# Optimization experiments

Hardware: AMD Instinct MI355X
Metric: run time of the kernel (lower is better)

The kernel has to match this reference:

```python
import jax, jax.numpy as jnp
import numpy as np

D_MODEL = 1024
D_STATE = 64


def setup_inputs() -> dict:
    key = jax.random.key(0)
    k_x, k_a, k_b, k_c, k_d = jax.random.split(key, 5)
    x = jax.random.normal(k_x, (4, 4096, D_MODEL), dtype=jnp.float32)
    # parameter init mirrors _init_parameters
    A_diag = jax.random.uniform(k_a, (D_STATE,), minval=-0.5, maxval=0.5, dtype=jnp.float32)
    def xavier(k, shape):
        fan_in, fan_out = shape
        limit = float(np.sqrt(6.0 / (fan_in + fan_out)))
        return jax.random.uniform(k, shape, minval=-limit, maxval=limit, dtype=jnp.float32)
    B = xavier(k_b, (D_MODEL, D_STATE))
    C = xavier(k_c, (D_STATE, D_MODEL))
    D = xavier(k_d, (D_MODEL, D_MODEL)) * 0.1
    return {"x": x, "A_diag": A_diag, "B": B, "C": C, "D": D}


def reference(x, A_diag, B, C, D):
    # h_t = sigmoid(A_diag) * h_{t-1} + x_t @ B ; y_t = h_t @ C + x_t @ D
    # dropout is identity in eval mode.
    a = jax.nn.sigmoid(A_diag)                      # [S_state]
    u = jnp.einsum('btd,ds->bts', x, B)             # precompute input drive [B,T,S]

    def step(h, u_t):                               # h: [B,S], u_t: [B,S]
        h = a * h + u_t
        return h, h

    h0 = jnp.zeros((x.shape[0], A_diag.shape[0]), dtype=x.dtype)
    _, hs = jax.lax.scan(step, h0, jnp.swapaxes(u, 0, 1))  # hs: [T,B,S]
    hs = jnp.swapaxes(hs, 0, 1)                            # [B,T,S]
    y = jnp.einsum('bts,sd->btd', hs, C) + jnp.einsum('btd,de->bte', x, D)
    return y
```

## Files before the change

kernel.cpp:

```cpp
#include <hip/hip_runtime.h>
#include <hip/hip_bf16.h>

using bf16x8 = __attribute__((ext_vector_type(8))) __bf16;
using f32x4  = __attribute__((ext_vector_type(4))) float;

#define MTOT   16384
#define DMODEL 1024
#define DSTATE 64
#define KBIG   1088

__device__ __forceinline__ ushort f2b(float f) {
  __hip_bfloat16 h = __float2bfloat16(f);
  return *reinterpret_cast<ushort*>(&h);
}

__device__ __forceinline__ void gld_lds16(const ushort* g, const char* l) {
  using gptr_t = const __attribute__((address_space(1))) uint32_t*;
  using lptr_t = __attribute__((address_space(3))) uint32_t*;
  __builtin_amdgcn_global_load_lds(
      reinterpret_cast<gptr_t>(reinterpret_cast<uintptr_t>(g)),
      reinterpret_cast<lptr_t>(static_cast<uint32_t>(reinterpret_cast<uintptr_t>(l))),
      16, 0, 0);
}

#define BARRIER() do { asm volatile("" ::: "memory"); __builtin_amdgcn_s_barrier(); asm volatile("" ::: "memory"); } while (0)
#define VMCNT4() asm volatile("s_waitcnt vmcnt(4)" ::: "memory")
#define VMCNT0() asm volatile("s_waitcnt vmcnt(0)" ::: "memory")

__global__ void prep_params(const float* __restrict__ A_diag, const float* __restrict__ B,
                            const float* __restrict__ C, const float* __restrict__ D,
                            ushort* __restrict__ Wt, ushort* __restrict__ Btu,
                            float* __restrict__ aSig) {
  int i = blockIdx.x * blockDim.x + threadIdx.x;
  int stride = gridDim.x * blockDim.x;
  for (int idx = i; idx < DMODEL * KBIG; idx += stride) {
    int n = idx / KBIG, k = idx % KBIG;
    float v = (k < DSTATE) ? C[k * DMODEL + n] : D[(size_t)(k - DSTATE) * DMODEL + n];
    Wt[idx] = f2b(v);
  }
  for (int idx = i; idx < DSTATE * DMODEL; idx += stride) {
    int s = idx >> 10, k = idx & 1023;
    Btu[idx] = f2b(B[k * DSTATE + s]);
  }
  if (i < DSTATE) aSig[i] = 1.0f / (1.0f + expf(-A_diag[i]));
}

__global__ __launch_bounds__(256) void fused_xu(const float* __restrict__ x,
    const ushort* __restrict__ Btu, const float* __restrict__ aSig,
    ushort* __restrict__ Z, float* __restrict__ Uloc, float* __restrict__ carry) {
  __shared__ ushort As[64][136];
  __shared__ float  Ul[64][68];
  int tid = threadIdx.x;
  int w = tid >> 6, lane = tid & 63;
  int l16 = lane & 15, lh = lane >> 4;
  int row0 = blockIdx.x * 64;

  f32x4 acc[4] = {};
  float4 xv[8];
#pragma unroll
  for (int p = 0; p < 8; ++p) {
    int fi = p * 256 + tid;
    int r = fi >> 5, kq = fi & 31;
    xv[p] = *reinterpret_cast<const float4*>(x + (size_t)(row0 + r) * 1024 + kq * 4);
  }
  for (int c = 0; c < 8; ++c) {
    int k0 = c * 128;
#pragma unroll
    for (int p = 0; p < 8; ++p) {
      int fi = p * 256 + tid;
      int r = fi >> 5, kq = fi & 31;
      ushort4 o;
      o.x = f2b(xv[p].x); o.y = f2b(xv[p].y); o.z = f2b(xv[p].z); o.w = f2b(xv[p].w);
      *reinterpret_cast<ushort4*>(&Z[(size_t)(row0 + r) * KBIG + DSTATE + k0 + kq * 4]) = o;
      *reinterpret_cast<ushort4*>(&As[r][kq * 4]) = o;
    }
    __syncthreads();
    if (c < 7) {
      int k1 = k0 + 128;
#pragma unroll
      for (int p = 0; p < 8; ++p) {
        int fi = p * 256 + tid;
        int r = fi >> 5, kq = fi & 31;
        xv[p] = *reinterpret_cast<const float4*>(x + (size_t)(row0 + r) * 1024 + k1 + kq * 4);
      }
    }
#pragma unroll
    for (int ks = 0; ks < 4; ++ks) {
      bf16x8 af = *reinterpret_cast<const bf16x8*>(&As[w * 16 + l16][ks * 32 + lh * 8]);
#pragma unroll
      for (int n = 0; n < 4; ++n) {
        bf16x8 bf = *reinterpret_cast<const bf16x8*>(
            &Btu[(size_t)(n * 16 + l16) * 1024 + k0 + ks * 32 + lh * 8]);
        acc[n] = __builtin_amdgcn_mfma_f32_16x16x32_bf16(af, bf, acc[n], 0, 0, 0);
      }
    }
    __syncthreads();
  }
#pragma unroll
  for (int n = 0; n < 4; ++n)
#pragma unroll
    for (int j = 0; j < 4; ++j)
      Ul[w * 16 + lh * 4 + j][n * 16 + l16] = acc[n][j];
  __syncthreads();
  int s = lane;
  float as = aSig[s];
  float h = 0.0f;
  int g = blockIdx.x * 4 + w;
#pragma unroll
  for (int i = 0; i < 16; ++i) {
    h = fmaf(as, h, Ul[w * 16 + i][s]);
    Uloc[(size_t)(g * 16 + i) * 64 + s] = h;
  }
  carry[(size_t)g * 64 + s] = h;
}

__global__ __launch_bounds__(256) void carry_scan(const float* __restrict__ aSig,
    const float* __restrict__ carry, float* __restrict__ Hpref) {
  int b = threadIdx.x >> 6, s = threadIdx.x & 63;
  float as = aSig[s];
  float aL = as;
#pragma unroll
  for (int q = 0; q < 4; ++q) aL *= aL;
  const float* cb = carry + ((size_t)b * 256) * 64 + s;
  float* hp = Hpref + ((size_t)b * 256) * 64 + s;
  float H = 0.0f;
  for (int c0 = 0; c0 < 256; c0 += 16) {
    float v[16];
#pragma unroll
    for (int i = 0; i < 16; ++i) v[i] = cb[(size_t)(c0 + i) * 64];
#pragma unroll
    for (int i = 0; i < 16; ++i) {
      hp[(size_t)(c0 + i) * 64] = H;
      H = fmaf(aL, H, v[i]);
    }
  }
}

__global__ __launch_bounds__(256) void scan_fix2(const float* __restrict__ aSig,
    const float* __restrict__ Uloc, const float* __restrict__ Hpref,
    ushort* __restrict__ Z) {
  int w = threadIdx.x >> 6, s = threadIdx.x & 63;
  int g = blockIdx.x * 4 + w;
  float as = aSig[s];
  float H = Hpref[(size_t)g * 64 + s];
  float p = as;
  size_t ubase = (size_t)g * 16 * 64 + s;
  size_t zbase = (size_t)(g * 16) * KBIG + s;
#pragma unroll
  for (int i = 0; i < 16; ++i) {
    float h = fmaf(p, H, Uloc[ubase + (size_t)i * 64]);
    p *= as;
    Z[zbase + (size_t)i * KBIG] = f2b(h);
  }
}

__global__ __launch_bounds__(512) void gemm256(const ushort* __restrict__ A, int lda,
                                               const ushort* __restrict__ Bt, int ldb,
                                               float* __restrict__ Cc, int ldc, int K) {
  extern __shared__ __align__(128) char smem[];
  const int tid = threadIdx.x;
  const int wid = tid >> 6, lane = tid & 63;
  const int wm = wid >> 2, wn = wid & 3;
  const int l16 = lane & 15, lh = lane >> 4;

  int bid = blockIdx.x;
  int swz = (bid & 7) * ((int)gridDim.x >> 3) + (bid >> 3);
  const int bmRow = (swz >> 2) * 256;
  const int bnCol = (swz & 3) * 256;

  const int NT = K / 64;

  const int cswz = ((lh ^ (l16 & 7)) << 4);
  const int sRow = lane >> 3;
  const int sCol = (((lane & 7) ^ (lane >> 3)) << 3);

  f32x4 acc[8][4] = {};
  bf16x8 aR[8], bR[8];

  auto stageA = [&](int buf, int t, int h) {
    size_t r = (size_t)(bmRow + h * 128 + wid * 8 + sRow);
    const ushort* g0 = A + r * (size_t)lda + t * 64 + sCol;
    const char* d = smem + buf * 65536 + (h * 128 + wid * 8) * 128;
    gld_lds16(g0, d);
    gld_lds16(g0 + (size_t)64 * lda, d + 64 * 128);
  };
  auto stageB = [&](int buf, int t, int h) {
    size_t r = (size_t)(bnCol + h * 128 + wid * 8 + sRow);
    const ushort* g0 = Bt + r * (size_t)ldb + t * 64 + sCol;
    const char* d = smem + buf * 65536 + 32768 + (h * 128 + wid * 8) * 128;
    gld_lds16(g0, d);
    gld_lds16(g0 + (size_t)64 * ldb, d + 64 * 128);
  };
  auto loadA = [&](int buf, int qm) {
#pragma unroll
    for (int m = 0; m < 4; ++m)
#pragma unroll
      for (int ks = 0; ks < 2; ++ks)
        aR[m * 2 + ks] = *reinterpret_cast<const bf16x8*>(
            smem + buf * 65536 + (wm * 128 + qm * 64 + m * 16 + l16) * 128 + (cswz ^ (ks * 64)));
  };
  auto loadB = [&](int buf, int qn) {
#pragma unroll
    for (int n = 0; n < 2; ++n)
#pragma unroll
      for (int ks = 0; ks < 2; ++ks)
        bR[qn * 4 + n * 2 + ks] = *reinterpret_cast<const bf16x8*>(
            smem + buf * 65536 + 32768 + (wn * 64 + qn * 32 + n * 16 + l16) * 128 + (cswz ^ (ks * 64)));
  };
  auto mfmaQ = [&](int qm, int qn) {
    __builtin_amdgcn_s_setprio(1);
    __builtin_amdgcn_sched_barrier(0);
#pragma unroll
    for (int ks = 0; ks < 2; ++ks)
#pragma unroll
      for (int m = 0; m < 4; ++m)
#pragma unroll
        for (int n = 0; n < 2; ++n)
          acc[qm * 4 + m][qn * 2 + n] = __builtin_amdgcn_mfma_f32_16x16x32_bf16(
              aR[m * 2 + ks], bR[qn * 4 + n * 2 + ks], acc[qm * 4 + m][qn * 2 + n], 0, 0, 0);
    __builtin_amdgcn_sched_barrier(0);
    __builtin_amdgcn_s_setprio(0);
  };

  stageA(0, 0, 0); stageA(0, 0, 1); stageB(0, 0, 0); stageB(0, 0, 1);
  if (1 < NT) { stageA(1, 1, 0); stageA(1, 1, 1); stageB(1, 1, 0); stageB(1, 1, 1); }
  VMCNT0();
  BARRIER();

  for (int t = 0; t < NT; t += 2) {
    const bool s01 = (t > 0) && (t + 1 < NT);
    const bool s23 = (t + 2 < NT);
    const bool s67 = (t + 3 < NT);
    loadA(0, 0); loadB(0, 0);
    if (s01) stageA(1, t + 1, 0);
    BARRIER(); mfmaQ(0, 0); BARRIER();
    loadB(0, 1);
    if (s01) stageA(1, t + 1, 1);
    BARRIER(); mfmaQ(0, 1); BARRIER();
    loadA(0, 1);
    if (s23) stageB(0, t + 2, 0);
    BARRIER(); mfmaQ(1, 0); BARRIER();
    if (s23) stageB(0, t + 2, 1);
    BARRIER(); mfmaQ(1, 1);
    if (s23) { VMCNT4(); } else { VMCNT0(); }
    BARRIER();
    if (t + 1 < NT) {
      loadA(1, 0); loadB(1, 0);
      if (s23) stageA(0, t + 2, 0);
      BARRIER(); mfmaQ(0, 0); BARRIER();
      loadB(1, 1);
      if (s23) stageA(0, t + 2, 1);
      BARRIER(); mfmaQ(0, 1); BARRIER();
      loadA(1, 1);
      if (s67) stageB(1, t + 3, 0);
      BARRIER(); mfmaQ(1, 0); BARRIER();
      if (s67) stageB(1, t + 3, 1);
      BARRIER(); mfmaQ(1, 1);
      if (s67) { VMCNT4(); } else { VMCNT0(); }
      BARRIER();
    }
  }

#pragma unroll
  for (int i = 0; i < 8; ++i)
#pragma unroll
    for (int jn = 0; jn < 4; ++jn)
#pragma unroll
      for (int j = 0; j < 4; ++j) {
        int r = bmRow + wm * 128 + (i >> 2) * 64 + (i & 3) * 16 + lh * 4 + j;
        int c = bnCol + wn * 64 + (jn >> 1) * 32 + (jn & 1) * 16 + l16;
        Cc[(size_t)r * ldc + c] = acc[i][jn][j];
      }
}

extern "C" void kernel_launch(void* const* d_in, const int* in_sizes, int n_in,
                              void* d_out, int out_size, void* d_ws, size_t ws_size,
                              hipStream_t stream) {
  const float* x      = (const float*)d_in[0];
  const float* A_diag = (const float*)d_in[1];
  const float* B      = (const float*)d_in[2];
  const float* C      = (const float*)d_in[3];
  const float* D      = (const float*)d_in[4];
  float* y = (float*)d_out;

  char* w = (char*)d_ws;
  ushort* Z     = (ushort*)(w);
  ushort* Wt    = (ushort*)(w + 35651584);
  ushort* Btu   = (ushort*)(w + 37879808);
  float*  Uloc  = (float*) (w + 38010880);
  float*  carry = (float*) (w + 42205184);
  float*  Hpref = (float*) (w + 42467328);
  float*  aSig  = (float*) (w + 42729472);

  (void)hipFuncSetAttribute(reinterpret_cast<const void*>(&gemm256),
                            hipFuncAttributeMaxDynamicSharedMemorySize, 131072);

  prep_params<<<dim3(1024), dim3(256), 0, stream>>>(A_diag, B, C, D, Wt, Btu, aSig);
  fused_xu<<<dim3(256), dim3(256), 0, stream>>>(x, Btu, aSig, Z, Uloc, carry);
  carry_scan<<<dim3(1), dim3(256), 0, stream>>>(aSig, carry, Hpref);
  scan_fix2<<<dim3(256), dim3(256), 0, stream>>>(aSig, Uloc, Hpref, Z);
  gemm256<<<dim3(64 * 4), dim3(512), 131072, stream>>>(Z, KBIG, Wt, KBIG, y, DMODEL, KBIG);
}
```

Before: 89.11 us.

## Restructure GEMM main loop with register-double-buffered fragments and fewer barriers

Rewrites the gemm256 main loop as a per-tile routine with two barriers per K-tile instead of about eight. The A and B LDS fragments are double-buffered in registers, so the next tile's fragments load while the current quadrant's MFMAs run. Staging now issues four global-to-LDS loads per operand in one block, the prologue waits only on the first buffer, and the sched_barrier fences are dropped so the compiler can interleave. This costs more VGPRs for the extra fragment buffers. The loop's tail handling assumes an odd tile count (K=1088 gives 17), so an even K would read the wrong buffer in the last tile.

```diff
diff --git a/kernel.cpp b/kernel.cpp
--- a/kernel.cpp
+++ b/kernel.cpp
@@ -24,6 +24,7 @@
 }
 
 #define BARRIER() do { asm volatile("" ::: "memory"); __builtin_amdgcn_s_barrier(); asm volatile("" ::: "memory"); } while (0)
+#define VMCNT8() asm volatile("s_waitcnt vmcnt(8)" ::: "memory")
 #define VMCNT4() asm volatile("s_waitcnt vmcnt(4)" ::: "memory")
 #define VMCNT0() asm volatile("s_waitcnt vmcnt(0)" ::: "memory")
 
@@ -171,45 +172,49 @@
   const int NT = K / 64;
 
   const int cswz = ((lh ^ (l16 & 7)) << 4);
+  const int sCol = (((lane & 7) ^ (lane >> 3)) << 3);
   const int sRow = lane >> 3;
-  const int sCol = (((lane & 7) ^ (lane >> 3)) << 3);
+
+  const ushort* aBase = A + (size_t)(bmRow + wid * 8 + sRow) * lda + sCol;
+  const ushort* bBase = Bt + (size_t)(bnCol + wid * 8 + sRow) * ldb + sCol;
+  char* aDst0 = smem + (wid * 8) * 128;
+  char* bDst0 = smem + 32768 + (wid * 8) * 128;
 
   f32x4 acc[8][4] = {};
-  bf16x8 aR[8], bR[8];
-
-  auto stageA = [&](int buf, int t, int h) {
-    size_t r = (size_t)(bmRow + h * 128 + wid * 8 + sRow);
-    const ushort* g0 = A + r * (size_t)lda + t * 64 + sCol;
-    const char* d = smem + buf * 65536 + (h * 128 + wid * 8) * 128;
-    gld_lds16(g0, d);
-    gld_lds16(g0 + (size_t)64 * lda, d + 64 * 128);
-  };
-  auto stageB = [&](int buf, int t, int h) {
-    size_t r = (size_t)(bnCol + h * 128 + wid * 8 + sRow);
-    const ushort* g0 = Bt + r * (size_t)ldb + t * 64 + sCol;
-    const char* d = smem + buf * 65536 + 32768 + (h * 128 + wid * 8) * 128;
-    gld_lds16(g0, d);
-    gld_lds16(g0 + (size_t)64 * ldb, d + 64 * 128);
-  };
-  auto loadA = [&](int buf, int qm) {
+  bf16x8 aQ0[8], aQ1[8], bQ0[4], bQ1[4];
+
+  auto stageA = [&](int buf, int t) {
+    const ushort* g = aBase + (size_t)t * 64;
+    char* d = aDst0 + buf * 65536;
+#pragma unroll
+    for (int h = 0; h < 4; ++h)
+      gld_lds16(g + (size_t)(h * 64) * lda, d + h * 64 * 128);
+  };
+  auto stageB = [&](int buf, int t) {
+    const ushort* g = bBase + (size_t)t * 64;
+    char* d = bDst0 + buf * 65536;
+#pragma unroll
+    for (int h = 0; h < 4; ++h)
+      gld_lds16(g + (size_t)(h * 64) * ldb, d + h * 64 * 128);
+  };
+  auto loadAq = [&](bf16x8 (&dst)[8], int buf, int qm) {
 #pragma unroll
     for (int m = 0; m < 4; ++m)
 #pragma unroll
       for (int ks = 0; ks < 2; ++ks)
-        aR[m * 2 + ks] = *reinterpret_cast<const bf16x8*>(
+        dst[m * 2 + ks] = *reinterpret_cast<const bf16x8*>(
             smem + buf * 65536 + (wm * 128 + qm * 64 + m * 16 + l16) * 128 + (cswz ^ (ks * 64)));
   };
-  auto loadB = [&](int buf, int qn) {
+  auto loadBq = [&](bf16x8 (&dst)[4], int buf, int qn) {
 #pragma unroll
     for (int n = 0; n < 2; ++n)
 #pragma unroll
       for (int ks = 0; ks < 2; ++ks)
-        bR[qn * 4 + n * 2 + ks] = *reinterpret_cast<const bf16x8*>(
+        dst[n * 2 + ks] = *reinterpret_cast<const bf16x8*>(
             smem + buf * 65536 + 32768 + (wn * 64 + qn * 32 + n * 16 + l16) * 128 + (cswz ^ (ks * 64)));
   };
-  auto mfmaQ = [&](int qm, int qn) {
+  auto mfmaQ = [&](bf16x8 (&a8)[8], bf16x8 (&b4)[4], int qm, int qn) {
     __builtin_amdgcn_s_setprio(1);
-    __builtin_amdgcn_sched_barrier(0);
 #pragma unroll
     for (int ks = 0; ks < 2; ++ks)
 #pragma unroll
@@ -217,49 +222,36 @@
 #pragma unroll
         for (int n = 0; n < 2; ++n)
           acc[qm * 4 + m][qn * 2 + n] = __builtin_amdgcn_mfma_f32_16x16x32_bf16(
-              aR[m * 2 + ks], bR[qn * 4 + n * 2 + ks], acc[qm * 4 + m][qn * 2 + n], 0, 0, 0);
-    __builtin_amdgcn_sched_barrier(0);
+              a8[m * 2 + ks], b4[n * 2 + ks], acc[qm * 4 + m][qn * 2 + n], 0, 0, 0);
     __builtin_amdgcn_s_setprio(0);
   };
 
-  stageA(0, 0, 0); stageA(0, 0, 1); stageB(0, 0, 0); stageB(0, 0, 1);
-  if (1 < NT) { stageA(1, 1, 0); stageA(1, 1, 1); stageB(1, 1, 0); stageB(1, 1, 1); }
-  VMCNT0();
+  auto tile = [&](int buf, int t, bool stage2, bool next) {
+    loadBq(bQ1, buf, 1);
+    mfmaQ(aQ0, bQ0, 0, 0);
+    loadAq(aQ1, buf, 1);
+    mfmaQ(aQ0, bQ1, 0, 1);
+    BARRIER();
+    if (stage2) stageB(buf, t + 2);
+    mfmaQ(aQ1, bQ0, 1, 0);
+    if (stage2) { VMCNT4(); } else { VMCNT0(); }
+    BARRIER();
+    if (stage2) stageA(buf, t + 2);
+    if (next) { loadAq(aQ0, buf ^ 1, 0); loadBq(bQ0, buf ^ 1, 0); }
+    mfmaQ(aQ1, bQ1, 1, 1);
+  };
+
+  stageA(0, 0); stageB(0, 0);
+  stageA(1, 1); stageB(1, 1);
+  VMCNT8();
   BARRIER();
-
-  for (int t = 0; t < NT; t += 2) {
-    const bool s01 = (t > 0) && (t + 1 < NT);
-    const bool s23 = (t + 2 < NT);
-    const bool s67 = (t + 3 < NT);
-    loadA(0, 0); loadB(0, 0);
-    if (s01) stageA(1, t + 1, 0);
-    BARRIER(); mfmaQ(0, 0); BARRIER();
-    loadB(0, 1);
-    if (s01) stageA(1, t + 1, 1);
-    BARRIER(); mfmaQ(0, 1); BARRIER();
-    loadA(0, 1);
-    if (s23) stageB(0, t + 2, 0);
-    BARRIER(); mfmaQ(1, 0); BARRIER();
-    if (s23) stageB(0, t + 2, 1);
-    BARRIER(); mfmaQ(1, 1);
-    if (s23) { VMCNT4(); } else { VMCNT0(); }
-    BARRIER();
-    if (t + 1 < NT) {
-      loadA(1, 0); loadB(1, 0);
-      if (s23) stageA(0, t + 2, 0);
-      BARRIER(); mfmaQ(0, 0); BARRIER();
-      loadB(1, 1);
-      if (s23) stageA(0, t + 2, 1);
-      BARRIER(); mfmaQ(0, 1); BARRIER();
-      loadA(1, 1);
-      if (s67) stageB(1, t + 3, 0);
-      BARRIER(); mfmaQ(1, 0); BARRIER();
-      if (s67) stageB(1, t + 3, 1);
-      BARRIER(); mfmaQ(1, 1);
-      if (s67) { VMCNT4(); } else { VMCNT0(); }
-      BARRIER();
-    }
-  }
+  loadAq(aQ0, 0, 0); loadBq(bQ0, 0, 0);
+
+  for (int t = 0; t + 1 < NT - 1; t += 2) {
+    tile(0, t,     t + 2 < NT, true);
+    tile(1, t + 1, t + 3 < NT, true);
+  }
+  tile(0, NT - 1, false, false);
 
 #pragma unroll
   for (int i = 0; i < 8; ++i)
```

Result: slower. 154.4 us (+73.3%).
